# Performance work log

Measured on AMD Instinct MI355X. Metric: run time of the kernel, lower is better.

The kernel has to match this reference:

```python
import jax, jax.numpy as jnp
import numpy as np
import math

B, LQ, D = 4, 1024, 2048
H, G = 16, 4            # n_heads, n_groups
HD = D // H             # 128
GS = H // G             # group_size = 4
PAST = 1024
LK = PAST + LQ
NEG = jnp.float32(-1e30)


def _rope(x, cos, sin):
    # x: [B, L, nh, HD]; cos/sin: [1, L, 1, HD//2]; llama-style complex rotation
    x1 = x[..., 0::2]
    x2 = x[..., 1::2]
    r1 = x1 * cos - x2 * sin
    r2 = x1 * sin + x2 * cos
    return jnp.stack([r1, r2], axis=-1).reshape(x.shape)


def setup_inputs() -> dict:
    key = jax.random.key(0)
    ks = jax.random.split(key, 12)
    s = 0.02
    x = jax.random.normal(ks[0], (B, LQ, D), jnp.float32)
    past_k = jax.random.normal(ks[1], (B, G, PAST, HD), jnp.float32)
    past_v = jax.random.normal(ks[2], (B, G, PAST, HD), jnp.float32)
    rotary_freqs = jax.random.uniform(ks[3], (LQ, HD // 2), jnp.float32) * 6.283
    # causal mask with cache: query i may attend to key j if j <= PAST + i
    q_pos = PAST + jnp.arange(LQ)[:, None]
    k_pos = jnp.arange(LK)[None, :]
    mask = (k_pos <= q_pos)  # [LQ, LK] bool
    Wq = jax.random.normal(ks[4], (D, D), jnp.float32) * s
    bq = jnp.zeros((D,), jnp.float32)
    Wk = jax.random.normal(ks[5], (D, G * HD), jnp.float32) * s
    bk = jnp.zeros((G * HD,), jnp.float32)
    Wv = jax.random.normal(ks[6], (D, G * HD), jnp.float32) * s
    bv = jnp.zeros((G * HD,), jnp.float32)
    Wo = jax.random.normal(ks[7], (D, D), jnp.float32) * s
    bo = jnp.zeros((D,), jnp.float32)
    return {"x": x, "mask": mask, "rotary_freqs": rotary_freqs,
            "past_k": past_k, "past_v": past_v,
            "Wq": Wq, "bq": bq, "Wk": Wk, "bk": bk,
            "Wv": Wv, "bv": bv, "Wo": Wo, "bo": bo}


def reference(x, mask, rotary_freqs, past_k, past_v, Wq, bq, Wk, bk, Wv, bv, Wo, bo):
    # projections (torch Linear math with weights stored [in, out])
    q = (x @ Wq + bq).reshape(B, LQ, H, HD)      # break_heads: [B,L,H,HD]
    k = (x @ Wk + bk).reshape(B, LQ, G, HD)      # [B,L,G,HD]
    v = (x @ Wv + bv).reshape(B, LQ, G, HD).transpose(0, 2, 1, 3)  # [B,G,L,HD]
    # RoPE on q,k then move heads forward (matches q.transpose(2,1))
    cos = jnp.cos(rotary_freqs)[None, :, None, :]
    sin = jnp.sin(rotary_freqs)[None, :, None, :]
    q = _rope(q, cos, sin).transpose(0, 2, 1, 3)  # [B,H,LQ,HD]
    k = _rope(k, cos, sin).transpose(0, 2, 1, 3)  # [B,G,LQ,HD]
    # KV cache append
    k = jnp.concatenate([past_k, k], axis=2)      # [B,G,LK,HD]
    v = jnp.concatenate([past_v, v], axis=2)
    # grouped-query attention
    qg = q.reshape(B, G, GS, LQ, HD)
    scores = jnp.einsum('bgsqd,bgkd->bgsqk', qg, k) / math.sqrt(HD)
    scores = jnp.where(mask[None, None, None, :, :], scores, NEG)
    att = jax.nn.softmax(scores, axis=-1)
    out = jnp.einsum('bgsqk,bgkd->bgsqd', att, v).reshape(B, H, LQ, HD)
    out = out.transpose(0, 2, 1, 3).reshape(B, LQ, D)  # concatenate_heads
    return out @ Wo + bo
```

## Files before the change

kernel.cpp:

```cpp
#include <hip/hip_runtime.h>

#define B_   4
#define LQ_  1024
#define D_   2048
#define H_   16
#define G_   4
#define HD_  128
#define GS_  4
#define PAST_ 1024
#define LK_  2048
#define NQKV 3072

typedef __attribute__((ext_vector_type(8))) short short8;
typedef __attribute__((ext_vector_type(4))) float f32x4;

__device__ __forceinline__ ushort f2b(float f) {
    unsigned u = __builtin_bit_cast(unsigned, f);
    u += 0x7FFF + ((u >> 16) & 1);
    return (ushort)(u >> 16);
}
__device__ __forceinline__ float b2f(ushort h) {
    unsigned u = ((unsigned)h) << 16;
    return __builtin_bit_cast(float, u);
}

#define GLD_LDS16(gp, lp) \
    __builtin_amdgcn_global_load_lds((__attribute__((address_space(1))) void*)(gp), \
                                     (__attribute__((address_space(3))) void*)(lp), 16, 0, 0)

__global__ __launch_bounds__(256) void prep_misc(const float* __restrict__ x,
                                                 ushort* __restrict__ xb,
                                                 const float* __restrict__ pk,
                                                 ushort* __restrict__ kc,
                                                 const float* __restrict__ bq,
                                                 const float* __restrict__ bk,
                                                 const float* __restrict__ bv,
                                                 float* __restrict__ bias) {
    int blk = blockIdx.x;
    int tid = threadIdx.x;
    if (blk < 8192) {
        int i = blk * 256 + tid;
        float4 v = ((const float4*)x)[i];
        ushort4 o;
        o.x = f2b(v.x); o.y = f2b(v.y); o.z = f2b(v.z); o.w = f2b(v.w);
        ((ushort4*)xb)[i] = o;
    } else if (blk < 10240) {
        int i = (blk - 8192) * 256 + tid;
        float4 v = ((const float4*)pk)[i];
        int bg  = i >> 15;
        int rem = i & 32767;
        ushort4 o;
        o.x = f2b(v.x); o.y = f2b(v.y); o.z = f2b(v.z); o.w = f2b(v.w);
        ((ushort4*)kc)[(size_t)bg * 65536 + rem] = o;
    } else {
        int i = (blk - 10240) * 256 + tid;
        if (i < 2048) bias[i] = bq[i];
        else if (i < 2560) bias[i] = bk[i - 2048];
        else if (i < 3072) bias[i] = bv[i - 2560];
    }
}

__global__ __launch_bounds__(256) void transpose_pack(const float* __restrict__ in,
                                                      ushort* __restrict__ out,
                                                      int rows_in, int cols_in,
                                                      long in_bstride, long out_bstride,
                                                      int out_rstride) {
    __shared__ float t[32][33];
    int bz = blockIdx.z;
    in  += (long)bz * in_bstride;
    out += (long)bz * out_bstride;
    int c0 = blockIdx.x * 32, r0 = blockIdx.y * 32;
    int tx = threadIdx.x, ty = threadIdx.y;
    #pragma unroll
    for (int i = 0; i < 32; i += 8) {
        int r = r0 + ty + i;
        if (r < rows_in && (c0 + tx) < cols_in)
            t[ty + i][tx] = in[(long)r * cols_in + c0 + tx];
    }
    __syncthreads();
    #pragma unroll
    for (int i = 0; i < 32; i += 8) {
        int c = c0 + ty + i, r = r0 + tx;
        if (c < cols_in && r < rows_in)
            out[(long)c * out_rstride + r] = f2b(t[tx][ty + i]);
    }
}

template <bool BF16_OUT>
__global__ __launch_bounds__(256) void gemm_bt(const ushort* __restrict__ A,
                                               const ushort* __restrict__ Bt,
                                               const float* __restrict__ bias,
                                               void* __restrict__ Cout,
                                               int M, int N, int K) {
    __shared__ ushort lA[128 * 32];
    __shared__ ushort lB[128 * 32];
    const int tid = threadIdx.x;
    const int wave = tid >> 6, lane = tid & 63;
    const int quad = lane >> 4, l15 = lane & 15;
    const int m0 = blockIdx.y * 128, n0 = blockIdx.x * 128;
    const int wm = (wave >> 1) * 64, wn = (wave & 1) * 64;

    f32x4 acc[4][4];
    #pragma unroll
    for (int i = 0; i < 4; ++i)
        #pragma unroll
        for (int j = 0; j < 4; ++j)
            #pragma unroll
            for (int r = 0; r < 4; ++r) acc[i][j][r] = 0.f;

    for (int k0 = 0; k0 < K; k0 += 32) {
        __syncthreads();
        #pragma unroll
        for (int i = 0; i < 2; ++i) {
            int chunk = wave * 2 + i;
            int flat = chunk * 512 + lane * 8;
            int row = flat >> 5, col = flat & 31;
            GLD_LDS16(A  + (size_t)(m0 + row) * K + k0 + col, lA + chunk * 512);
            GLD_LDS16(Bt + (size_t)(n0 + row) * K + k0 + col, lB + chunk * 512);
        }
        __syncthreads();
        short8 af[4], bf[4];
        #pragma unroll
        for (int i = 0; i < 4; ++i)
            af[i] = *(const short8*)(lA + (wm + i * 16 + l15) * 32 + quad * 8);
        #pragma unroll
        for (int j = 0; j < 4; ++j)
            bf[j] = *(const short8*)(lB + (wn + j * 16 + l15) * 32 + quad * 8);
        #pragma unroll
        for (int i = 0; i < 4; ++i)
            #pragma unroll
            for (int j = 0; j < 4; ++j)
                acc[i][j] = __builtin_amdgcn_mfma_f32_16x16x32_bf16(af[i], bf[j], acc[i][j], 0, 0, 0);
    }

    #pragma unroll
    for (int i = 0; i < 4; ++i)
        #pragma unroll
        for (int j = 0; j < 4; ++j)
            #pragma unroll
            for (int r = 0; r < 4; ++r) {
                int row = m0 + wm + i * 16 + quad * 4 + r;
                int col = n0 + wn + j * 16 + l15;
                float v = acc[i][j][r] + bias[col];
                if (BF16_OUT) ((ushort*)Cout)[(size_t)row * N + col] = f2b(v);
                else          ((float*)Cout)[(size_t)row * N + col] = v;
            }
}

__global__ __launch_bounds__(256) void rope_pack(const ushort* __restrict__ qkvb,
                                                 const float* __restrict__ rf,
                                                 ushort* __restrict__ qb,
                                                 ushort* __restrict__ kc,
                                                 ushort* __restrict__ vtc) {
    const float SC = 0.08838834764831845f;
    int row = blockIdx.x;
    int b = row >> 10, qi = row & 1023;
    int tid = threadIdx.x;
    const ushort* src = qkvb + (size_t)row * NQKV;

    for (int p = tid; p < 1024; p += 256) {
        int h = p >> 6, i = p & 63;
        float fr = rf[qi * 64 + i];
        float s, c; __sincosf(fr, &s, &c);
        uint pr = *(const uint*)(src + h * 128 + 2 * i);
        float x1 = b2f((ushort)(pr & 0xffff));
        float x2 = b2f((ushort)(pr >> 16));
        float r1 = (x1 * c - x2 * s) * SC;
        float r2 = (x1 * s + x2 * c) * SC;
        size_t o = (((size_t)(b * H_ + h)) * LQ_ + qi) * HD_ + 2 * i;
        *(uint*)(qb + o) = (uint)f2b(r1) | ((uint)f2b(r2) << 16);
    }
    {
        int g = tid >> 6, i = tid & 63;
        float fr = rf[qi * 64 + i];
        float s, c; __sincosf(fr, &s, &c);
        uint pr = *(const uint*)(src + 2048 + g * 128 + 2 * i);
        float x1 = b2f((ushort)(pr & 0xffff));
        float x2 = b2f((ushort)(pr >> 16));
        float r1 = x1 * c - x2 * s;
        float r2 = x1 * s + x2 * c;
        size_t o = (((size_t)(b * G_ + g)) * LK_ + PAST_ + qi) * HD_ + 2 * i;
        *(uint*)(kc + o) = (uint)f2b(r1) | ((uint)f2b(r2) << 16);
    }
    for (int e = tid; e < 512; e += 256) {
        int g = e >> 7, d = e & 127;
        vtc[(((size_t)(b * G_ + g)) * HD_ + d) * LK_ + PAST_ + qi] = src[2560 + e];
    }
}

__global__ __launch_bounds__(256, 2) void attn_kernel(const ushort* __restrict__ qb,
                                                      const ushort* __restrict__ kc,
                                                      const ushort* __restrict__ vtc,
                                                      ushort* __restrict__ attn_a) {
    __shared__ ushort kt[2][64 * 128];
    __shared__ ushort vtt[2][128 * 64];
    __shared__ ushort pt[4 * 32 * 64];

    const int tid = threadIdx.x;
    const int wave = tid >> 6, lane = tid & 63;
    const int quad = lane >> 4, l15 = lane & 15;
    const int q0 = blockIdx.x * 128;
    const int bh = blockIdx.y;
    const int b = bh >> 4, h = bh & 15, g = h >> 2;
    const ushort* kcb = kc + ((size_t)(b * G_ + g)) * LK_ * HD_;
    const ushort* vcb = vtc + ((size_t)(b * G_ + g)) * HD_ * LK_;

    int ksrc[4], vsrc[4];
    #pragma unroll
    for (int i = 0; i < 4; ++i) {
        int u = (wave * 4 + i) * 64 + lane;
        int key = u >> 4, cs = u & 15;
        ksrc[i] = key * HD_ + ((cs ^ (key & 15)) << 3);
        int d = u >> 3, c2 = u & 7;
        vsrc[i] = d * LK_ + ((c2 ^ (d & 7)) << 3);
    }

    short8 qf[2][4];
    #pragma unroll
    for (int qfr = 0; qfr < 2; ++qfr) {
        int qrow = q0 + wave * 32 + qfr * 16 + l15;
        const ushort* qp = qb + (((size_t)(b * H_ + h)) * LQ_ + qrow) * HD_ + quad * 8;
        #pragma unroll
        for (int kk = 0; kk < 4; ++kk) qf[qfr][kk] = *(const short8*)(qp + kk * 32);
    }

    f32x4 o[2][8];
    #pragma unroll
    for (int qfr = 0; qfr < 2; ++qfr)
        #pragma unroll
        for (int f = 0; f < 8; ++f)
            #pragma unroll
            for (int r = 0; r < 4; ++r) o[qfr][f][r] = 0.f;
    float lst[2][4];
    #pragma unroll
    for (int qfr = 0; qfr < 2; ++qfr)
        #pragma unroll
        for (int r = 0; r < 4; ++r) lst[qfr][r] = 0.f;

    const int nsteps = (PAST_ + q0 + 128) >> 6;

    #pragma unroll
    for (int i = 0; i < 4; ++i) {
        int ci = wave * 4 + i;
        GLD_LDS16(kcb + ksrc[i], kt[0] + ci * 512);
        GLD_LDS16(vcb + vsrc[i], vtt[0] + ci * 512);
    }

    for (int it = 0; it < nsteps; ++it) {
        const int k0 = it << 6;
        const int cur = it & 1, nxt = cur ^ 1;
        __syncthreads();
        if (it + 1 < nsteps) {
            const int k1 = k0 + 64;
            #pragma unroll
            for (int i = 0; i < 4; ++i) {
                int ci = wave * 4 + i;
                GLD_LDS16(kcb + (size_t)k1 * HD_ + ksrc[i], kt[nxt] + ci * 512);
                GLD_LDS16(vcb + k1 + vsrc[i], vtt[nxt] + ci * 512);
            }
        }

        f32x4 z[2][4];
        #pragma unroll
        for (int qfr = 0; qfr < 2; ++qfr)
            #pragma unroll
            for (int kf = 0; kf < 4; ++kf)
                #pragma unroll
                for (int r = 0; r < 4; ++r) z[qfr][kf][r] = 0.f;
        #pragma unroll
        for (int kk = 0; kk < 4; ++kk) {
            #pragma unroll
            for (int kf = 0; kf < 4; ++kf) {
                int key = kf * 16 + l15;
                const short8 bk = *(const short8*)(kt[cur] + key * 128 + (((kk * 4 + quad) ^ l15) << 3));
                z[0][kf] = __builtin_amdgcn_mfma_f32_16x16x32_bf16(qf[0][kk], bk, z[0][kf], 0, 0, 0);
                z[1][kf] = __builtin_amdgcn_mfma_f32_16x16x32_bf16(qf[1][kk], bk, z[1][kf], 0, 0, 0);
            }
        }

        const bool mask_step = (it >= nsteps - 2);
        #pragma unroll
        for (int qfr = 0; qfr < 2; ++qfr) {
            #pragma unroll
            for (int kf = 0; kf < 4; ++kf) {
                #pragma unroll
                for (int r = 0; r < 4; ++r) {
                    int row = qfr * 16 + quad * 4 + r;
                    float pv_ = __expf(z[qfr][kf][r]);
                    if (mask_step) {
                        int qpos = PAST_ + q0 + wave * 32 + row;
                        if (k0 + kf * 16 + l15 > qpos) pv_ = 0.f;
                    }
                    lst[qfr][r] += pv_;
                    int col = kf * 16 + l15;
                    pt[wave * 2048 + row * 64 + ((((col >> 3) ^ (row & 7)) << 3) | (col & 7))] = f2b(pv_);
                }
            }
        }

        short8 pa[2][2];
        #pragma unroll
        for (int qfr = 0; qfr < 2; ++qfr) {
            int prow = qfr * 16 + l15;
            #pragma unroll
            for (int j = 0; j < 2; ++j)
                pa[qfr][j] = *(const short8*)(pt + wave * 2048 + prow * 64 + (((j * 4 + quad) ^ (prow & 7)) << 3));
        }
        #pragma unroll
        for (int f = 0; f < 8; ++f) {
            #pragma unroll
            for (int j = 0; j < 2; ++j) {
                int d = f * 16 + l15;
                const short8 bv = *(const short8*)(vtt[cur] + d * 64 + (((j * 4 + quad) ^ (l15 & 7)) << 3));
                o[0][f] = __builtin_amdgcn_mfma_f32_16x16x32_bf16(pa[0][j], bv, o[0][f], 0, 0, 0);
                o[1][f] = __builtin_amdgcn_mfma_f32_16x16x32_bf16(pa[1][j], bv, o[1][f], 0, 0, 0);
            }
        }
    }

    #pragma unroll
    for (int qfr = 0; qfr < 2; ++qfr) {
        float linv[4];
        #pragma unroll
        for (int r = 0; r < 4; ++r) {
            float rs = lst[qfr][r];
            rs += __shfl_xor(rs, 1);
            rs += __shfl_xor(rs, 2);
            rs += __shfl_xor(rs, 4);
            rs += __shfl_xor(rs, 8);
            linv[r] = 1.0f / rs;
        }
        #pragma unroll
        for (int f = 0; f < 8; ++f)
            #pragma unroll
            for (int r = 0; r < 4; ++r) {
                int q = q0 + wave * 32 + qfr * 16 + quad * 4 + r;
                int d = f * 16 + l15;
                attn_a[((size_t)(b * LQ_ + q)) * D_ + h * HD_ + d] = f2b(o[qfr][f][r] * linv[r]);
            }
    }
}


extern "C" void kernel_launch(void* const* d_in, const int* in_sizes, int n_in,
                              void* d_out, int out_size, void* d_ws, size_t ws_size,
                              hipStream_t stream) {
    const float* x  = (const float*)d_in[0];
    const float* rf = (const float*)d_in[2];
    const float* pk = (const float*)d_in[3];
    const float* pv = (const float*)d_in[4];
    const float* Wq = (const float*)d_in[5];
    const float* bq = (const float*)d_in[6];
    const float* Wk = (const float*)d_in[7];
    const float* bk = (const float*)d_in[8];
    const float* Wv = (const float*)d_in[9];
    const float* bv = (const float*)d_in[10];
    const float* Wo = (const float*)d_in[11];
    const float* bo = (const float*)d_in[12];
    float* out = (float*)d_out;

    char* p = (char*)d_ws;
    auto take = [&](size_t n) { void* r = p; p += (n + 255) & ~(size_t)255; return r; };
    ushort* xb       = (ushort*)take((size_t)4096 * 2048 * 2);
    ushort* wt_qkv   = (ushort*)take((size_t)3072 * 2048 * 2);
    ushort* wt_o     = (ushort*)take((size_t)2048 * 2048 * 2);
    float*  bias_qkv = (float*) take((size_t)3072 * 4);
    ushort* qkvb     = (ushort*)take((size_t)4096 * 3072 * 2);
    ushort* qb       = (ushort*)take((size_t)B_ * H_ * LQ_ * HD_ * 2);
    ushort* kcache   = (ushort*)take((size_t)B_ * G_ * LK_ * HD_ * 2);
    ushort* vtc      = (ushort*)take((size_t)B_ * G_ * HD_ * LK_ * 2);
    ushort* attn_a   = (ushort*)take((size_t)4096 * 2048 * 2);

    dim3 tb(32, 8);
    prep_misc<<<10252, 256, 0, stream>>>(x, xb, pk, kcache, bq, bk, bv, bias_qkv);
    transpose_pack<<<dim3(64, 64, 1), tb, 0, stream>>>(Wq, wt_qkv, 2048, 2048, 0, 0, 2048);
    transpose_pack<<<dim3(16, 64, 1), tb, 0, stream>>>(Wk, wt_qkv + (size_t)2048 * 2048, 2048, 512, 0, 0, 2048);
    transpose_pack<<<dim3(16, 64, 1), tb, 0, stream>>>(Wv, wt_qkv + (size_t)2560 * 2048, 2048, 512, 0, 0, 2048);
    transpose_pack<<<dim3(64, 64, 1), tb, 0, stream>>>(Wo, wt_o, 2048, 2048, 0, 0, 2048);
    transpose_pack<<<dim3(4, 32, 16), tb, 0, stream>>>(pv, vtc, 1024, 128,
                                                       (long)1024 * 128, (long)128 * 2048, 2048);

    gemm_bt<true><<<dim3(24, 32), 256, 0, stream>>>(xb, wt_qkv, bias_qkv, qkvb, 4096, 3072, 2048);
    rope_pack<<<4096, 256, 0, stream>>>(qkvb, rf, qb, kcache, vtc);
    attn_kernel<<<dim3(8, 64), 256, 0, stream>>>(qb, kcache, vtc, attn_a);
    gemm_bt<false><<<dim3(16, 32), 256, 0, stream>>>(attn_a, wt_o, bo, out, 4096, 2048, 2048);
}
```

Before: 407.6 us.

## Split attention waves 2x2 over queries and keys/dims with shared P tile

Reorganizes the attention block so waves form a 2x2 grid: each wave handles 64 query rows and half of the keys for QK^T, and half of the head dimension for PV. The P tile is shared across waves, which needs an extra barrier per step and a cross-wave row-sum reduction at the end. This is meant to cut the per-wave LDS reads of K and V fragments and raise MFMA reuse per load. It also reverses tile order for half the batch-heads to balance causal work, and raises wave priority around MFMA sections.

Result: no change. 405.3 us (-0.6%).

```diff
diff --git a/kernel.cpp b/kernel.cpp
--- a/kernel.cpp
+++ b/kernel.cpp
@@ -194,12 +194,15 @@
                                                       ushort* __restrict__ attn_a) {
     __shared__ ushort kt[2][64 * 128];
     __shared__ ushort vtt[2][128 * 64];
-    __shared__ ushort pt[4 * 32 * 64];
+    __shared__ ushort pt[128 * 64];
 
     const int tid = threadIdx.x;
     const int wave = tid >> 6, lane = tid & 63;
     const int quad = lane >> 4, l15 = lane & 15;
-    const int q0 = blockIdx.x * 128;
+    const int qh = wave >> 1;
+    const int jw = wave & 1;
+    const int tile = (blockIdx.y < 32) ? blockIdx.x : (7 - (int)blockIdx.x);
+    const int q0 = tile << 7;
     const int bh = blockIdx.y;
     const int b = bh >> 4, h = bh & 15, g = h >> 2;
     const ushort* kcb = kc + ((size_t)(b * G_ + g)) * LK_ * HD_;
@@ -215,25 +218,25 @@
         vsrc[i] = d * LK_ + ((c2 ^ (d & 7)) << 3);
     }
 
-    short8 qf[2][4];
-    #pragma unroll
-    for (int qfr = 0; qfr < 2; ++qfr) {
-        int qrow = q0 + wave * 32 + qfr * 16 + l15;
+    short8 qf[4][4];
+    #pragma unroll
+    for (int qfr = 0; qfr < 4; ++qfr) {
+        int qrow = q0 + qh * 64 + qfr * 16 + l15;
         const ushort* qp = qb + (((size_t)(b * H_ + h)) * LQ_ + qrow) * HD_ + quad * 8;
         #pragma unroll
         for (int kk = 0; kk < 4; ++kk) qf[qfr][kk] = *(const short8*)(qp + kk * 32);
     }
 
-    f32x4 o[2][8];
-    #pragma unroll
-    for (int qfr = 0; qfr < 2; ++qfr)
-        #pragma unroll
-        for (int f = 0; f < 8; ++f)
+    f32x4 o[4][4];
+    #pragma unroll
+    for (int qfr = 0; qfr < 4; ++qfr)
+        #pragma unroll
+        for (int f = 0; f < 4; ++f)
             #pragma unroll
             for (int r = 0; r < 4; ++r) o[qfr][f][r] = 0.f;
-    float lst[2][4];
-    #pragma unroll
-    for (int qfr = 0; qfr < 2; ++qfr)
+    float lst[4][4];
+    #pragma unroll
+    for (int qfr = 0; qfr < 4; ++qfr)
         #pragma unroll
         for (int r = 0; r < 4; ++r) lst[qfr][r] = 0.f;
 
@@ -260,70 +263,86 @@
             }
         }
 
-        f32x4 z[2][4];
-        #pragma unroll
-        for (int qfr = 0; qfr < 2; ++qfr)
-            #pragma unroll
-            for (int kf = 0; kf < 4; ++kf)
+        f32x4 z[4][2];
+        #pragma unroll
+        for (int qfr = 0; qfr < 4; ++qfr)
+            #pragma unroll
+            for (int kf = 0; kf < 2; ++kf)
                 #pragma unroll
                 for (int r = 0; r < 4; ++r) z[qfr][kf][r] = 0.f;
+        __builtin_amdgcn_s_setprio(1);
         #pragma unroll
         for (int kk = 0; kk < 4; ++kk) {
             #pragma unroll
-            for (int kf = 0; kf < 4; ++kf) {
-                int key = kf * 16 + l15;
+            for (int kf = 0; kf < 2; ++kf) {
+                int key = jw * 32 + kf * 16 + l15;
                 const short8 bk = *(const short8*)(kt[cur] + key * 128 + (((kk * 4 + quad) ^ l15) << 3));
-                z[0][kf] = __builtin_amdgcn_mfma_f32_16x16x32_bf16(qf[0][kk], bk, z[0][kf], 0, 0, 0);
-                z[1][kf] = __builtin_amdgcn_mfma_f32_16x16x32_bf16(qf[1][kk], bk, z[1][kf], 0, 0, 0);
-            }
-        }
+                #pragma unroll
+                for (int qfr = 0; qfr < 4; ++qfr)
+                    z[qfr][kf] = __builtin_amdgcn_mfma_f32_16x16x32_bf16(qf[qfr][kk], bk, z[qfr][kf], 0, 0, 0);
+            }
+        }
+        __builtin_amdgcn_s_setprio(0);
 
         const bool mask_step = (it >= nsteps - 2);
         #pragma unroll
-        for (int qfr = 0; qfr < 2; ++qfr) {
-            #pragma unroll
-            for (int kf = 0; kf < 4; ++kf) {
+        for (int qfr = 0; qfr < 4; ++qfr) {
+            #pragma unroll
+            for (int kf = 0; kf < 2; ++kf) {
                 #pragma unroll
                 for (int r = 0; r < 4; ++r) {
-                    int row = qfr * 16 + quad * 4 + r;
+                    int row = qh * 64 + qfr * 16 + quad * 4 + r;
+                    int col = jw * 32 + kf * 16 + l15;
                     float pv_ = __expf(z[qfr][kf][r]);
                     if (mask_step) {
-                        int qpos = PAST_ + q0 + wave * 32 + row;
-                        if (k0 + kf * 16 + l15 > qpos) pv_ = 0.f;
+                        int qpos = PAST_ + q0 + row;
+                        if (k0 + col > qpos) pv_ = 0.f;
                     }
                     lst[qfr][r] += pv_;
-                    int col = kf * 16 + l15;
-                    pt[wave * 2048 + row * 64 + ((((col >> 3) ^ (row & 7)) << 3) | (col & 7))] = f2b(pv_);
+                    pt[row * 64 + ((((col >> 3) ^ (row & 7)) << 3) | (col & 7))] = f2b(pv_);
                 }
             }
         }
 
-        short8 pa[2][2];
-        #pragma unroll
-        for (int qfr = 0; qfr < 2; ++qfr) {
-            int prow = qfr * 16 + l15;
-            #pragma unroll
-            for (int j = 0; j < 2; ++j)
-                pa[qfr][j] = *(const short8*)(pt + wave * 2048 + prow * 64 + (((j * 4 + quad) ^ (prow & 7)) << 3));
-        }
-        #pragma unroll
-        for (int f = 0; f < 8; ++f) {
-            #pragma unroll
-            for (int j = 0; j < 2; ++j) {
-                int d = f * 16 + l15;
-                const short8 bv = *(const short8*)(vtt[cur] + d * 64 + (((j * 4 + quad) ^ (l15 & 7)) << 3));
-                o[0][f] = __builtin_amdgcn_mfma_f32_16x16x32_bf16(pa[0][j], bv, o[0][f], 0, 0, 0);
-                o[1][f] = __builtin_amdgcn_mfma_f32_16x16x32_bf16(pa[1][j], bv, o[1][f], 0, 0, 0);
-            }
-        }
-    }
-
-    #pragma unroll
-    for (int qfr = 0; qfr < 2; ++qfr) {
+        asm volatile("s_waitcnt lgkmcnt(0)" ::: "memory");
+        __builtin_amdgcn_s_barrier();
+        __builtin_amdgcn_sched_barrier(0);
+
+        __builtin_amdgcn_s_setprio(1);
+        #pragma unroll
+        for (int j2 = 0; j2 < 2; ++j2) {
+            short8 pa[4];
+            #pragma unroll
+            for (int qfr = 0; qfr < 4; ++qfr) {
+                int prow = qh * 64 + qfr * 16 + l15;
+                pa[qfr] = *(const short8*)(pt + prow * 64 + (((j2 * 4 + quad) ^ (prow & 7)) << 3));
+            }
+            #pragma unroll
+            for (int f = 0; f < 4; ++f) {
+                int d = jw * 64 + f * 16 + l15;
+                const short8 bv = *(const short8*)(vtt[cur] + d * 64 + (((j2 * 4 + quad) ^ (l15 & 7)) << 3));
+                #pragma unroll
+                for (int qfr = 0; qfr < 4; ++qfr)
+                    o[qfr][f] = __builtin_amdgcn_mfma_f32_16x16x32_bf16(pa[qfr], bv, o[qfr][f], 0, 0, 0);
+            }
+        }
+        __builtin_amdgcn_s_setprio(0);
+    }
+
+    __syncthreads();
+    float* scr = (float*)pt;
+    #pragma unroll
+    for (int qfr = 0; qfr < 4; ++qfr)
+        #pragma unroll
+        for (int r = 0; r < 4; ++r)
+            scr[wave * 1024 + (qfr * 4 + r) * 64 + lane] = lst[qfr][r];
+    __syncthreads();
+    #pragma unroll
+    for (int qfr = 0; qfr < 4; ++qfr) {
         float linv[4];
         #pragma unroll
         for (int r = 0; r < 4; ++r) {
-            float rs = lst[qfr][r];
+            float rs = lst[qfr][r] + scr[(wave ^ 1) * 1024 + (qfr * 4 + r) * 64 + lane];
             rs += __shfl_xor(rs, 1);
             rs += __shfl_xor(rs, 2);
             rs += __shfl_xor(rs, 4);
@@ -331,11 +350,11 @@
             linv[r] = 1.0f / rs;
         }
         #pragma unroll
-        for (int f = 0; f < 8; ++f)
+        for (int f = 0; f < 4; ++f)
             #pragma unroll
             for (int r = 0; r < 4; ++r) {
-                int q = q0 + wave * 32 + qfr * 16 + quad * 4 + r;
-                int d = f * 16 + l15;
+                int q = q0 + qh * 64 + qfr * 16 + quad * 4 + r;
+                int d = jw * 64 + f * 16 + l15;
                 attn_a[((size_t)(b * LQ_ + q)) * D_ + h * HD_ + d] = f2b(o[qfr][f][r] * linv[r]);
             }
     }
```
